# Performance work log

Measured on AMD Instinct MI355X. Metric: run time of the kernel, lower is better.

Reference implementation:

```python
import jax, jax.numpy as jnp
import numpy as np

BN_EPS = 1e-5


def _gather_neighbors(feat, idx):
    # feat: [B, N, C]; idx: [B, N, K] -> [B, N, K, C]
    B, N, C = feat.shape
    K = idx.shape[-1]
    g = jnp.take_along_axis(feat, idx.reshape(B, N * K)[:, :, None], axis=1)
    return g.reshape(B, N, K, C)


def setup_inputs() -> dict:
    key = jax.random.key(0)
    k1, k2, k3 = jax.random.split(key, 3)
    B, C, N, K, Cout = 4, 128, 4096, 16, 256
    x = jax.random.normal(k1, (B, C, N, 1), dtype=jnp.float32)
    edge_index = jax.random.randint(k2, (2, B, N, K), 0, N, dtype=jnp.int64)
    # 1x1 conv weight [Cout, 2C] (kaiming-like scale), bias zeros (per reset_parameters)
    fan_in = 2 * C
    w = jax.random.normal(k3, (Cout, 2 * C), dtype=jnp.float32) * np.sqrt(2.0 / fan_in)
    b = jnp.zeros((Cout,), dtype=jnp.float32)
    gamma = jnp.ones((Cout,), dtype=jnp.float32)
    beta = jnp.zeros((Cout,), dtype=jnp.float32)
    return {"x": x, "w": w, "b": b, "gamma": gamma, "beta": beta,
            "edge_index": edge_index}


def reference(x, w, b, gamma, beta, edge_index):
    # x: [B, C, N, 1], edge_index: [2, B, N, K]
    B, C, N, _ = x.shape
    feat = jnp.transpose(x[:, :, :, 0], (0, 2, 1))            # [B, N, C]
    x_i = _gather_neighbors(feat, edge_index[1])              # [B, N, K, C]
    x_j = _gather_neighbors(feat, edge_index[0])              # [B, N, K, C]
    h = jnp.concatenate([x_i, x_j - x_i], axis=-1)            # [B, N, K, 2C]
    # 1x1 conv == per-position matmul
    y = jnp.einsum('bnkc,oc->bnko', h, w) + b                 # [B, N, K, Cout]
    y = jax.nn.relu(y)
    # BatchNorm2d (train mode): biased stats over (B, N, K) per channel
    mean = jnp.mean(y, axis=(0, 1, 2))
    var = jnp.mean(jnp.square(y), axis=(0, 1, 2)) - jnp.square(mean)
    y = (y - mean) * jax.lax.rsqrt(var + BN_EPS) * gamma + beta
    # max over neighbors K, keepdim on last torch dim
    out = jnp.max(y, axis=2)                                  # [B, N, Cout]
    return jnp.transpose(out, (0, 2, 1))[:, :, :, None]       # [B, Cout, N, 1]
```

## Files before the change

### kernel.cpp

```cpp
#include <hip/hip_runtime.h>
#include <hip/hip_bf16.h>

#define BB 4
#define CC 128
#define TWOC 256
#define NN 4096
#define KK 16
#define COUT 256
#define NPB 32
#define BNK (BB*NN*KK)
#define K1GRID ((BB*NN)/NPB)
#define NPAIR (NPB/2)

typedef __attribute__((ext_vector_type(8))) short short8;
typedef __attribute__((ext_vector_type(4))) float f32x4;

__device__ __forceinline__ short f2bs(float f) {
  union { __hip_bfloat16 h; short s; } u;
  u.h = __float2bfloat16(f);
  return u.s;
}
__device__ __forceinline__ float bs2f(unsigned short s) {
  union { unsigned int u; float f; } v;
  v.u = ((unsigned int)s) << 16;
  return v.f;
}

__global__ void __launch_bounds__(256) k0_transpose(const float* __restrict__ x,
                                                    unsigned short* __restrict__ featbf,
                                                    float* __restrict__ gsum,
                                                    float* __restrict__ gsq) {
  __shared__ float tile[64][129];
  int b = blockIdx.x >> 6;
  int n0 = (blockIdx.x & 63) << 6;
  int t = threadIdx.x;
  if (blockIdx.x == 0) { gsum[t] = 0.f; gsq[t] = 0.f; }
#pragma unroll
  for (int i = 0; i < 32; ++i) {
    int flat = t + i * 256;
    int c = flat >> 6;
    int nl = flat & 63;
    tile[nl][c] = x[((size_t)(b * CC + c) * NN) + n0 + nl];
  }
  __syncthreads();
#pragma unroll
  for (int i = 0; i < 8; ++i) {
    int e = t + i * 256;
    int c4 = (e & 31) << 2;
    int nl = e >> 5;
    ushort4 u;
    u.x = (unsigned short)f2bs(tile[nl][c4 + 0]);
    u.y = (unsigned short)f2bs(tile[nl][c4 + 1]);
    u.z = (unsigned short)f2bs(tile[nl][c4 + 2]);
    u.w = (unsigned short)f2bs(tile[nl][c4 + 3]);
    *(ushort4*)(featbf + ((size_t)(b * NN + n0 + nl) * CC + c4)) = u;
  }
}

__global__ void __launch_bounds__(512, 4) k1_main(
    const unsigned short* __restrict__ featbf,
    const float* __restrict__ w, const float* __restrict__ bias,
    const int* __restrict__ eidx,
    unsigned short* __restrict__ nmaxh, unsigned short* __restrict__ nminh,
    float* __restrict__ gsum, float* __restrict__ gsq)
{
  __shared__ short hsh[2][32 * 256];
  const int tid = threadIdx.x;
  const int wv   = tid >> 6;
  const int lane = tid & 63;
  const int l15  = lane & 15;
  const int lhi  = lane >> 4;
  const int colbase = wv * 32;

  short8 bfrag[8][2];
#pragma unroll
  for (int t = 0; t < 8; ++t)
#pragma unroll
    for (int ct = 0; ct < 2; ++ct) {
      int col = colbase + ct * 16 + l15;
      int k0 = t * 32 + lhi * 8;
      const float* wr = w + (size_t)col * TWOC + k0;
      short8 f;
#pragma unroll
      for (int j = 0; j < 8; ++j) f[j] = f2bs(wr[j]);
      bfrag[t][ct] = f;
    }
  float biasv[2];
#pragma unroll
  for (int ct = 0; ct < 2; ++ct) biasv[ct] = bias[colbase + ct * 16 + l15];

  float cs[2] = {0.f, 0.f};
  float cq[2] = {0.f, 0.f};

  const int rr  = tid >> 4;
  const int c8  = (tid & 15) * 8;
  const int swz = (rr & 7) << 4;

  const int g0 = blockIdx.x * NPB;
  const int b  = g0 >> 12;
  const int n0 = g0 & (NN - 1);
  const unsigned short* fb = featbf + (size_t)b * NN * CC;
  const int* e0 = eidx + ((b * NN + n0) * KK + rr);
  const int* e1 = e0 + BNK;

  auto stage = [&](char* hb, uint4 Fi, uint4 Fj) {
    *(uint4*)(hb + (((rr * 256 + c8) * 2) ^ swz)) = Fi;
    uint4 d;
    unsigned int* pi = (unsigned int*)&Fi;
    unsigned int* pj = (unsigned int*)&Fj;
    unsigned int* pd = (unsigned int*)&d;
#pragma unroll
    for (int q = 0; q < 4; ++q) {
      float lo = bs2f((unsigned short)(pj[q] & 0xffff)) - bs2f((unsigned short)(pi[q] & 0xffff));
      float hi = bs2f((unsigned short)(pj[q] >> 16))    - bs2f((unsigned short)(pi[q] >> 16));
      pd[q] = ((unsigned int)(unsigned short)f2bs(lo)) |
              (((unsigned int)(unsigned short)f2bs(hi)) << 16);
    }
    *(uint4*)(hb + (((rr * 256 + 128 + c8) * 2) ^ swz)) = d;
  };

  uint4 fi, fj;

  {
    int ij = e0[0], ii = e1[0];
    uint4 Fj = *(const uint4*)(fb + (size_t)ij * CC + c8);
    uint4 Fi = *(const uint4*)(fb + (size_t)ii * CC + c8);
    stage((char*)hsh[0], Fi, Fj);
    int ij1 = e0[32], ii1 = e1[32];
    fj = *(const uint4*)(fb + (size_t)ij1 * CC + c8);
    fi = *(const uint4*)(fb + (size_t)ii1 * CC + c8);
  }
  __syncthreads();

  const int asw = (l15 & 7) << 4;

  for (int p = 0; p < NPAIR; ++p) {
    char* hb = (char*)hsh[p & 1];
    char* hn = (char*)hsh[(p & 1) ^ 1];

    int ij2 = 0, ii2 = 0;
    if (p + 2 < NPAIR) { ij2 = e0[(p + 2) * 32]; ii2 = e1[(p + 2) * 32]; }

    f32x4 acc[2][2] = {};
#pragma unroll
    for (int nl = 0; nl < 2; ++nl) {
      const int rbase = (nl * 16 + l15) * 256;
#pragma unroll
      for (int t = 0; t < 8; ++t) {
        short8 a = *(short8*)(hb + (((rbase + t * 32 + lhi * 8) * 2) ^ asw));
        acc[nl][0] = __builtin_amdgcn_mfma_f32_16x16x32_bf16(a, bfrag[t][0], acc[nl][0], 0, 0, 0);
        acc[nl][1] = __builtin_amdgcn_mfma_f32_16x16x32_bf16(a, bfrag[t][1], acc[nl][1], 0, 0, 0);
      }
    }

    if (p + 1 < NPAIR) {
      stage(hn, fi, fj);
      if (p + 2 < NPAIR) {
        fj = *(const uint4*)(fb + (size_t)ij2 * CC + c8);
        fi = *(const uint4*)(fb + (size_t)ii2 * CC + c8);
      }
    }

#pragma unroll
    for (int nl = 0; nl < 2; ++nl) {
      const int g = g0 + 2 * p + nl;
#pragma unroll
      for (int ct = 0; ct < 2; ++ct) {
        float vmax = -1e30f, vmin = 1e30f, vs = 0.f, vq = 0.f;
#pragma unroll
        for (int i = 0; i < 4; ++i) {
          float v = acc[nl][ct][i] + biasv[ct];
          v = fmaxf(v, 0.f);
          vmax = fmaxf(vmax, v);
          vmin = fminf(vmin, v);
          vs += v;
          vq += v * v;
        }
        cs[ct] += vs;
        cq[ct] += vq;
        vmax = fmaxf(vmax, __shfl_xor(vmax, 16));
        vmax = fmaxf(vmax, __shfl_xor(vmax, 32));
        vmin = fminf(vmin, __shfl_xor(vmin, 16));
        vmin = fminf(vmin, __shfl_xor(vmin, 32));
        if (lane < 16) {
          int col = colbase + ct * 16 + l15;
          nmaxh[(size_t)g * COUT + col] = (unsigned short)f2bs(vmax);
          nminh[(size_t)g * COUT + col] = (unsigned short)f2bs(vmin);
        }
      }
    }
    __syncthreads();
  }

#pragma unroll
  for (int ct = 0; ct < 2; ++ct) {
    float s = cs[ct], q = cq[ct];
    s += __shfl_xor(s, 16);  s += __shfl_xor(s, 32);
    q += __shfl_xor(q, 16);  q += __shfl_xor(q, 32);
    if (lane < 16) {
      int col = colbase + ct * 16 + l15;
      atomicAdd(&gsum[col], s);
      atomicAdd(&gsq[col], q);
    }
  }
}

__global__ void __launch_bounds__(256) k2_out(const unsigned short* __restrict__ nmaxh,
                                              const unsigned short* __restrict__ nminh,
                                              const float* __restrict__ gsum,
                                              const float* __restrict__ gsq,
                                              const float* __restrict__ gamma,
                                              const float* __restrict__ beta,
                                              float* __restrict__ out) {
  __shared__ float tile[COUT][33];
  int b = blockIdx.x >> 7;
  int n0 = (blockIdx.x & 127) << 5;
  int t = threadIdx.x;
  const float inv = 1.0f / (float)BNK;
  float mean = gsum[t] * inv;
  float var  = gsq[t] * inv - mean * mean;
  float sc = gamma[t] * rsqrtf(var + 1e-5f);
  float sh = beta[t] - mean * sc;
  const unsigned short* src = (sc >= 0.f) ? nmaxh : nminh;
#pragma unroll
  for (int rr = 0; rr < 32; ++rr) {
    size_t g = (size_t)(b * NN + n0 + rr) * COUT + t;
    tile[t][rr] = bs2f(src[g]) * sc + sh;
  }
  __syncthreads();
#pragma unroll
  for (int i = 0; i < 32; ++i) {
    int o = i * 8 + (t >> 5);
    int nl = t & 31;
    out[((size_t)(b * COUT + o) * NN) + n0 + nl] = tile[o][nl];
  }
}

extern "C" void kernel_launch(void* const* d_in, const int* in_sizes, int n_in,
                              void* d_out, int out_size, void* d_ws, size_t ws_size,
                              hipStream_t stream) {
  const float* x     = (const float*)d_in[0];
  const float* w     = (const float*)d_in[1];
  const float* bias  = (const float*)d_in[2];
  const float* gamma = (const float*)d_in[3];
  const float* beta  = (const float*)d_in[4];
  const int*   eidx  = (const int*)d_in[5];

  char* ws = (char*)d_ws;
  unsigned short* featbf = (unsigned short*)(ws);
  unsigned short* nmaxh  = (unsigned short*)(ws + 4194304);
  unsigned short* nminh  = (unsigned short*)(ws + 12582912);
  float* gsum   = (float*)(ws + 20971520);
  float* gsq    = (float*)(ws + 20972544);
  float* out = (float*)d_out;

  k0_transpose<<<256, 256, 0, stream>>>(x, featbf, gsum, gsq);
  k1_main<<<K1GRID, 512, 0, stream>>>(featbf, w, bias, eidx, nmaxh, nminh, gsum, gsq);
  k2_out<<<512, 256, 0, stream>>>(nmaxh, nminh, gsum, gsq, gamma, beta, out);
}
```

Before: 157.9 us.

## Retile main kernel into 256x128 LDS-staged MFMA tiles with prepacked bf16 weights

The main kernel is restructured. Each block now handles 16 points (256 edge rows) and one half of the output channels, with the bf16 weight half staged in LDS instead of held in registers. The weights are converted to bf16 once in the transpose kernel. Each wave computes a 64x64 tile over two K phases (x_i, then x_j−x_i) using 128KB of dynamic LDS, replacing the per-pair double-buffered loop. This raises MFMA reuse per LDS load and cuts the per-block weight conversion, but the large LDS footprint limits occupancy to one block per CU and the gather latency is no longer overlapped with compute.

New measurement: 207.6 us. 31.5% more time.

```diff
diff --git a/kernel.cpp b/kernel.cpp
--- a/kernel.cpp
+++ b/kernel.cpp
@@ -7,10 +7,9 @@
 #define NN 4096
 #define KK 16
 #define COUT 256
-#define NPB 32
 #define BNK (BB*NN*KK)
-#define K1GRID ((BB*NN)/NPB)
-#define NPAIR (NPB/2)
+#define NPB 16
+#define K1GRID (((BB*NN)/NPB)*2)
 
 typedef __attribute__((ext_vector_type(8))) short short8;
 typedef __attribute__((ext_vector_type(4))) float f32x4;
@@ -28,6 +27,8 @@
 
 __global__ void __launch_bounds__(256) k0_transpose(const float* __restrict__ x,
                                                     unsigned short* __restrict__ featbf,
+                                                    const float* __restrict__ w,
+                                                    unsigned short* __restrict__ wbf,
                                                     float* __restrict__ gsum,
                                                     float* __restrict__ gsq) {
   __shared__ float tile[64][129];
@@ -35,6 +36,7 @@
   int n0 = (blockIdx.x & 63) << 6;
   int t = threadIdx.x;
   if (blockIdx.x == 0) { gsum[t] = 0.f; gsq[t] = 0.f; }
+  wbf[blockIdx.x * 256 + t] = (unsigned short)f2bs(w[blockIdx.x * 256 + t]);
 #pragma unroll
   for (int i = 0; i < 32; ++i) {
     int flat = t + i * 256;
@@ -57,57 +59,99 @@
   }
 }
 
-__global__ void __launch_bounds__(512, 4) k1_main(
+__global__ void __launch_bounds__(512, 1) k1_main(
     const unsigned short* __restrict__ featbf,
-    const float* __restrict__ w, const float* __restrict__ bias,
+    const unsigned short* __restrict__ wbf,
+    const float* __restrict__ bias,
     const int* __restrict__ eidx,
     unsigned short* __restrict__ nmaxh, unsigned short* __restrict__ nminh,
     float* __restrict__ gsum, float* __restrict__ gsq)
 {
-  __shared__ short hsh[2][32 * 256];
-  const int tid = threadIdx.x;
+  extern __shared__ char lds[];
+  char* sB = lds;
+  char* sA = lds + 65536;
+
+  const int tid  = threadIdx.x;
+  const int lane = tid & 63;
   const int wv   = tid >> 6;
-  const int lane = tid & 63;
   const int l15  = lane & 15;
   const int lhi  = lane >> 4;
-  const int colbase = wv * 32;
-
-  short8 bfrag[8][2];
-#pragma unroll
-  for (int t = 0; t < 8; ++t)
-#pragma unroll
-    for (int ct = 0; ct < 2; ++ct) {
-      int col = colbase + ct * 16 + l15;
-      int k0 = t * 32 + lhi * 8;
-      const float* wr = w + (size_t)col * TWOC + k0;
-      short8 f;
-#pragma unroll
-      for (int j = 0; j < 8; ++j) f[j] = f2bs(wr[j]);
-      bfrag[t][ct] = f;
-    }
-  float biasv[2];
-#pragma unroll
-  for (int ct = 0; ct < 2; ++ct) biasv[ct] = bias[colbase + ct * 16 + l15];
-
-  float cs[2] = {0.f, 0.f};
-  float cq[2] = {0.f, 0.f};
-
-  const int rr  = tid >> 4;
-  const int c8  = (tid & 15) * 8;
-  const int swz = (rr & 7) << 4;
-
-  const int g0 = blockIdx.x * NPB;
-  const int b  = g0 >> 12;
-  const int n0 = g0 & (NN - 1);
+  const int wr   = wv >> 1;
+  const int wc   = wv & 1;
+
+  const int mt  = (int)blockIdx.x >> 1;
+  const int chf = (int)blockIdx.x & 1;
+  const int g0  = mt * NPB;
+  const int b   = g0 >> 12;
+  const int n0  = g0 & (NN - 1);
   const unsigned short* fb = featbf + (size_t)b * NN * CC;
-  const int* e0 = eidx + ((b * NN + n0) * KK + rr);
-  const int* e1 = e0 + BNK;
-
-  auto stage = [&](char* hb, uint4 Fi, uint4 Fj) {
-    *(uint4*)(hb + (((rr * 256 + c8) * 2) ^ swz)) = Fi;
+
+  {
+    const int col = tid >> 2;
+    const int kb  = (tid & 3) * 64;
+    const unsigned short* src = wbf + (size_t)(chf * 128 + col) * TWOC + kb;
+    const int ab = col * 512 + kb * 2;
+    const int sw = (col & 7) << 4;
+#pragma unroll
+    for (int j = 0; j < 8; ++j)
+      *(uint4*)(sB + ((ab + j * 16) ^ sw)) = *(const uint4*)((const char*)src + j * 16);
+  }
+
+  const int r0 = tid >> 4;
+  const int ch = tid & 15;
+  int idxi[8], idxj[8];
+#pragma unroll
+  for (int p = 0; p < 8; ++p) {
+    int row = r0 + 32 * p;
+    int ebase = (b * NN + n0 + (row >> 4)) * KK + (row & 15);
+    idxj[p] = eidx[ebase];
+    idxi[p] = eidx[BNK + ebase];
+  }
+  uint4 fi[8];
+#pragma unroll
+  for (int p = 0; p < 8; ++p)
+    fi[p] = *(const uint4*)(fb + (size_t)idxi[p] * CC + ch * 8);
+#pragma unroll
+  for (int p = 0; p < 8; ++p) {
+    int row = r0 + 32 * p;
+    *(uint4*)(sA + ((row * 256 + ch * 16) ^ ((row & 7) << 4))) = fi[p];
+  }
+  uint4 fj[8];
+#pragma unroll
+  for (int p = 0; p < 8; ++p)
+    fj[p] = *(const uint4*)(fb + (size_t)idxj[p] * CC + ch * 8);
+
+  __syncthreads();
+
+  f32x4 acc[4][4] = {};
+  const int asw = (l15 & 7) << 4;
+
+#pragma unroll
+  for (int kk = 0; kk < 4; ++kk) {
+    short8 a[4], bg[4];
+#pragma unroll
+    for (int rt = 0; rt < 4; ++rt) {
+      int row = wr * 64 + rt * 16 + l15;
+      a[rt] = *(short8*)(sA + ((row * 256 + kk * 64 + lhi * 16) ^ asw));
+    }
+#pragma unroll
+    for (int ct = 0; ct < 4; ++ct) {
+      int col = wc * 64 + ct * 16 + l15;
+      bg[ct] = *(short8*)(sB + ((col * 512 + kk * 64 + lhi * 16) ^ asw));
+    }
+#pragma unroll
+    for (int rt = 0; rt < 4; ++rt)
+#pragma unroll
+      for (int ct = 0; ct < 4; ++ct)
+        acc[rt][ct] = __builtin_amdgcn_mfma_f32_16x16x32_bf16(a[rt], bg[ct], acc[rt][ct], 0, 0, 0);
+  }
+  __syncthreads();
+
+#pragma unroll
+  for (int p = 0; p < 8; ++p) {
     uint4 d;
-    unsigned int* pi = (unsigned int*)&Fi;
-    unsigned int* pj = (unsigned int*)&Fj;
+    unsigned int* pi = (unsigned int*)&fi[p];
+    unsigned int* pj = (unsigned int*)&fj[p];
     unsigned int* pd = (unsigned int*)&d;
 #pragma unroll
     for (int q = 0; q < 4; ++q) {
@@ -116,89 +160,69 @@
       pd[q] = ((unsigned int)(unsigned short)f2bs(lo)) |
               (((unsigned int)(unsigned short)f2bs(hi)) << 16);
     }
-    *(uint4*)(hb + (((rr * 256 + 128 + c8) * 2) ^ swz)) = d;
-  };
-
-  uint4 fi, fj;
-
-  {
-    int ij = e0[0], ii = e1[0];
-    uint4 Fj = *(const uint4*)(fb + (size_t)ij * CC + c8);
-    uint4 Fi = *(const uint4*)(fb + (size_t)ii * CC + c8);
-    stage((char*)hsh[0], Fi, Fj);
-    int ij1 = e0[32], ii1 = e1[32];
-    fj = *(const uint4*)(fb + (size_t)ij1 * CC + c8);
-    fi = *(const uint4*)(fb + (size_t)ii1 * CC + c8);
-  }
-  __syncthreads();
-
-  const int asw = (l15 & 7) << 4;
-
-  for (int p = 0; p < NPAIR; ++p) {
-    char* hb = (char*)hsh[p & 1];
-    char* hn = (char*)hsh[(p & 1) ^ 1];
-
-    int ij2 = 0, ii2 = 0;
-    if (p + 2 < NPAIR) { ij2 = e0[(p + 2) * 32]; ii2 = e1[(p + 2) * 32]; }
-
-    f32x4 acc[2][2] = {};
-#pragma unroll
-    for (int nl = 0; nl < 2; ++nl) {
-      const int rbase = (nl * 16 + l15) * 256;
-#pragma unroll
-      for (int t = 0; t < 8; ++t) {
-        short8 a = *(short8*)(hb + (((rbase + t * 32 + lhi * 8) * 2) ^ asw));
-        acc[nl][0] = __builtin_amdgcn_mfma_f32_16x16x32_bf16(a, bfrag[t][0], acc[nl][0], 0, 0, 0);
-        acc[nl][1] = __builtin_amdgcn_mfma_f32_16x16x32_bf16(a, bfrag[t][1], acc[nl][1], 0, 0, 0);
+    int row = r0 + 32 * p;
+    *(uint4*)(sA + ((row * 256 + ch * 16) ^ ((row & 7) << 4))) = d;
+  }
+  __syncthreads();
+
+#pragma unroll
+  for (int kk = 0; kk < 4; ++kk) {
+    short8 a[4], bg[4];
+#pragma unroll
+    for (int rt = 0; rt < 4; ++rt) {
+      int row = wr * 64 + rt * 16 + l15;
+      a[rt] = *(short8*)(sA + ((row * 256 + kk * 64 + lhi * 16) ^ asw));
+    }
+#pragma unroll
+    for (int ct = 0; ct < 4; ++ct) {
+      int col = wc * 64 + ct * 16 + l15;
+      bg[ct] = *(short8*)(sB + ((col * 512 + 256 + kk * 64 + lhi * 16) ^ asw));
+    }
+#pragma unroll
+    for (int rt = 0; rt < 4; ++rt)
+#pragma unroll
+      for (int ct = 0; ct < 4; ++ct)
+        acc[rt][ct] = __builtin_amdgcn_mfma_f32_16x16x32_bf16(a[rt], bg[ct], acc[rt][ct], 0, 0, 0);
+  }
+
+  float biasv[4];
+#pragma unroll
+  for (int ct = 0; ct < 4; ++ct) biasv[ct] = bias[chf * 128 + wc * 64 + ct * 16 + l15];
+
+  float cs[4] = {0.f, 0.f, 0.f, 0.f};
+  float cq[4] = {0.f, 0.f, 0.f, 0.f};
+#pragma unroll
+  for (int rt = 0; rt < 4; ++rt) {
+    const int g = g0 + wr * 4 + rt;
+#pragma unroll
+    for (int ct = 0; ct < 4; ++ct) {
+      float vmax = -1e30f, vmin = 1e30f;
+#pragma unroll
+      for (int i = 0; i < 4; ++i) {
+        float v = fmaxf(acc[rt][ct][i] + biasv[ct], 0.f);
+        vmax = fmaxf(vmax, v);
+        vmin = fminf(vmin, v);
+        cs[ct] += v;
+        cq[ct] += v * v;
       }
-    }
-
-    if (p + 1 < NPAIR) {
-      stage(hn, fi, fj);
-      if (p + 2 < NPAIR) {
-        fj = *(const uint4*)(fb + (size_t)ij2 * CC + c8);
-        fi = *(const uint4*)(fb + (size_t)ii2 * CC + c8);
+      vmax = fmaxf(vmax, __shfl_xor(vmax, 16));
+      vmax = fmaxf(vmax, __shfl_xor(vmax, 32));
+      vmin = fminf(vmin, __shfl_xor(vmin, 16));
+      vmin = fminf(vmin, __shfl_xor(vmin, 32));
+      if (lane < 16) {
+        int col = chf * 128 + wc * 64 + ct * 16 + l15;
+        nmaxh[(size_t)g * COUT + col] = (unsigned short)f2bs(vmax);
+        nminh[(size_t)g * COUT + col] = (unsigned short)f2bs(vmin);
       }
     }
-
-#pragma unroll
-    for (int nl = 0; nl < 2; ++nl) {
-      const int g = g0 + 2 * p + nl;
-#pragma unroll
-      for (int ct = 0; ct < 2; ++ct) {
-        float vmax = -1e30f, vmin = 1e30f, vs = 0.f, vq = 0.f;
-#pragma unroll
-        for (int i = 0; i < 4; ++i) {
-          float v = acc[nl][ct][i] + biasv[ct];
-          v = fmaxf(v, 0.f);
-          vmax = fmaxf(vmax, v);
-          vmin = fminf(vmin, v);
-          vs += v;
-          vq += v * v;
-        }
-        cs[ct] += vs;
-        cq[ct] += vq;
-        vmax = fmaxf(vmax, __shfl_xor(vmax, 16));
-        vmax = fmaxf(vmax, __shfl_xor(vmax, 32));
-        vmin = fminf(vmin, __shfl_xor(vmin, 16));
-        vmin = fminf(vmin, __shfl_xor(vmin, 32));
-        if (lane < 16) {
-          int col = colbase + ct * 16 + l15;
-          nmaxh[(size_t)g * COUT + col] = (unsigned short)f2bs(vmax);
-          nminh[(size_t)g * COUT + col] = (unsigned short)f2bs(vmin);
-        }
-      }
-    }
-    __syncthreads();
-  }
-
-#pragma unroll
-  for (int ct = 0; ct < 2; ++ct) {
+  }
+#pragma unroll
+  for (int ct = 0; ct < 4; ++ct) {
     float s = cs[ct], q = cq[ct];
     s += __shfl_xor(s, 16);  s += __shfl_xor(s, 32);
     q += __shfl_xor(q, 16);  q += __shfl_xor(q, 32);
     if (lane < 16) {
-      int col = colbase + ct * 16 + l15;
+      int col = chf * 128 + wc * 64 + ct * 16 + l15;
       atomicAdd(&gsum[col], s);
       atomicAdd(&gsq[col], q);
     }
@@ -248,13 +272,14 @@
 
   char* ws = (char*)d_ws;
   unsigned short* featbf = (unsigned short*)(ws);
-  unsigned short* nmaxh  = (unsigned short*)(ws + 4194304);
-  unsigned short* nminh  = (unsigned short*)(ws + 12582912);
-  float* gsum   = (float*)(ws + 20971520);
-  float* gsq    = (float*)(ws + 20972544);
+  unsigned short* wbf    = (unsigned short*)(ws + 4194304);
+  unsigned short* nmaxh  = (unsigned short*)(ws + 4325376);
+  unsigned short* nminh  = (unsigned short*)(ws + 12713984);
+  float* gsum = (float*)(ws + 21102592);
+  float* gsq  = (float*)(ws + 21103616);
   float* out = (float*)d_out;
 
-  k0_transpose<<<256, 256, 0, stream>>>(x, featbf, gsum, gsq);
-  k1_main<<<K1GRID, 512, 0, stream>>>(featbf, w, bias, eidx, nmaxh, nminh, gsum, gsq);
+  k0_transpose<<<256, 256, 0, stream>>>(x, featbf, w, wbf, gsum, gsq);
+  k1_main<<<K1GRID, 512, 131072, stream>>>(featbf, wbf, bias, eidx, nmaxh, nminh, gsum, gsq);
   k2_out<<<512, 256, 0, stream>>>(nmaxh, nminh, gsum, gsq, gamma, beta, out);
 }
```

## Fold edge difference into weights and feed gathered rows directly to MFMA

Applied to the files above, without the earlier changes.

Rewrites the conv as W1·x_i + W2·x_j, with W1 = Wl − Wr and W2 = Wr precomputed in bf16 during the prep kernel. This removes the per-edge subtraction and the LDS staging buffer. Each lane now loads gathered feature rows from global memory straight into MFMA operand registers, double-buffered in registers, so there are no block-wide barriers. Each block handles 64 nodes with 16 lanes covering 4 nodes × 4 neighbors per MFMA tile, and launch bounds drop to 2 blocks per CU; register pressure from the operand buffers and the scattered 16-byte global gathers are the risk.

After: 206.6 us. 30.9% more time.

```diff
diff --git a/kernel.cpp b/kernel.cpp
--- a/kernel.cpp
+++ b/kernel.cpp
@@ -7,34 +7,48 @@
 #define NN 4096
 #define KK 16
 #define COUT 256
-#define NPB 32
 #define BNK (BB*NN*KK)
-#define K1GRID ((BB*NN)/NPB)
-#define NPAIR (NPB/2)
+#define NODES (BB*NN)
+#define NPB 64
+#define NGRP (NPB/4)
+#define NIT (NGRP*4)
+#define K1GRID (NODES/NPB)
 
 typedef __attribute__((ext_vector_type(8))) short short8;
 typedef __attribute__((ext_vector_type(4))) float f32x4;
 
-__device__ __forceinline__ short f2bs(float f) {
+static __device__ __forceinline__ short f2bs(float f) {
   union { __hip_bfloat16 h; short s; } u;
   u.h = __float2bfloat16(f);
   return u.s;
 }
-__device__ __forceinline__ float bs2f(unsigned short s) {
+static __device__ __forceinline__ float bs2f(unsigned short s) {
   union { unsigned int u; float f; } v;
   v.u = ((unsigned int)s) << 16;
   return v.f;
 }
 
-__global__ void __launch_bounds__(256) k0_transpose(const float* __restrict__ x,
-                                                    unsigned short* __restrict__ featbf,
-                                                    float* __restrict__ gsum,
-                                                    float* __restrict__ gsq) {
+__global__ void __launch_bounds__(256) k0_prep(const float* __restrict__ x,
+                                               unsigned short* __restrict__ featbf,
+                                               const float* __restrict__ w,
+                                               unsigned short* __restrict__ w1c,
+                                               unsigned short* __restrict__ w2c,
+                                               float* __restrict__ gsum,
+                                               float* __restrict__ gsq) {
   __shared__ float tile[64][129];
   int b = blockIdx.x >> 6;
   int n0 = (blockIdx.x & 63) << 6;
   int t = threadIdx.x;
   if (blockIdx.x == 0) { gsum[t] = 0.f; gsq[t] = 0.f; }
+  {
+    int col = blockIdx.x;
+    if (t < CC) {
+      float wl = w[col * TWOC + t];
+      float wr = w[col * TWOC + CC + t];
+      w1c[col * CC + t] = (unsigned short)f2bs(wl - wr);
+      w2c[col * CC + t] = (unsigned short)f2bs(wr);
+    }
+  }
 #pragma unroll
   for (int i = 0; i < 32; ++i) {
     int flat = t + i * 256;
@@ -57,150 +71,124 @@
   }
 }
 
-__global__ void __launch_bounds__(512, 4) k1_main(
+__global__ void __launch_bounds__(512, 2) k1_main(
     const unsigned short* __restrict__ featbf,
-    const float* __restrict__ w, const float* __restrict__ bias,
+    const unsigned short* __restrict__ w1c,
+    const unsigned short* __restrict__ w2c,
+    const float* __restrict__ bias,
     const int* __restrict__ eidx,
     unsigned short* __restrict__ nmaxh, unsigned short* __restrict__ nminh,
     float* __restrict__ gsum, float* __restrict__ gsq)
 {
-  __shared__ short hsh[2][32 * 256];
-  const int tid = threadIdx.x;
+  const int tid  = threadIdx.x;
   const int wv   = tid >> 6;
   const int lane = tid & 63;
   const int l15  = lane & 15;
   const int lhi  = lane >> 4;
   const int colbase = wv * 32;
 
-  short8 bfrag[8][2];
-#pragma unroll
-  for (int t = 0; t < 8; ++t)
+  const int g0 = blockIdx.x * NPB;
+  const int b  = g0 >> 12;
+  const unsigned short* fbb = featbf + ((size_t)b * NN) * CC;
+
+  short8 w1f[4][2], w2f[4][2];
+#pragma unroll
+  for (int t = 0; t < 4; ++t)
 #pragma unroll
     for (int ct = 0; ct < 2; ++ct) {
       int col = colbase + ct * 16 + l15;
-      int k0 = t * 32 + lhi * 8;
-      const float* wr = w + (size_t)col * TWOC + k0;
-      short8 f;
-#pragma unroll
-      for (int j = 0; j < 8; ++j) f[j] = f2bs(wr[j]);
-      bfrag[t][ct] = f;
-    }
-  float biasv[2];
-#pragma unroll
-  for (int ct = 0; ct < 2; ++ct) biasv[ct] = bias[colbase + ct * 16 + l15];
+      w1f[t][ct] = *(const short8*)(w1c + (size_t)col * CC + t * 32 + lhi * 8);
+      w2f[t][ct] = *(const short8*)(w2c + (size_t)col * CC + t * 32 + lhi * 8);
+    }
+  float biasv[2] = { bias[colbase + l15], bias[colbase + 16 + l15] };
 
   float cs[2] = {0.f, 0.f};
   float cq[2] = {0.f, 0.f};
-
-  const int rr  = tid >> 4;
-  const int c8  = (tid & 15) * 8;
-  const int swz = (rr & 7) << 4;
-
-  const int g0 = blockIdx.x * NPB;
-  const int b  = g0 >> 12;
-  const int n0 = g0 & (NN - 1);
-  const unsigned short* fb = featbf + (size_t)b * NN * CC;
-  const int* e0 = eidx + ((b * NN + n0) * KK + rr);
+  float vmax[2], vmin[2];
+
+  const int nl4 = l15 >> 2;
+  const int kq  = l15 & 3;
+  const int* e0 = eidx + ((size_t)g0 * KK + nl4 * KK + kq);
   const int* e1 = e0 + BNK;
-
-  auto stage = [&](char* hb, uint4 Fi, uint4 Fj) {
-    *(uint4*)(hb + (((rr * 256 + c8) * 2) ^ swz)) = Fi;
-    uint4 d;
-    unsigned int* pi = (unsigned int*)&Fi;
-    unsigned int* pj = (unsigned int*)&Fj;
-    unsigned int* pd = (unsigned int*)&d;
-#pragma unroll
-    for (int q = 0; q < 4; ++q) {
-      float lo = bs2f((unsigned short)(pj[q] & 0xffff)) - bs2f((unsigned short)(pi[q] & 0xffff));
-      float hi = bs2f((unsigned short)(pj[q] >> 16))    - bs2f((unsigned short)(pi[q] >> 16));
-      pd[q] = ((unsigned int)(unsigned short)f2bs(lo)) |
-              (((unsigned int)(unsigned short)f2bs(hi)) << 16);
-    }
-    *(uint4*)(hb + (((rr * 256 + 128 + c8) * 2) ^ swz)) = d;
+  auto qoff = [&](int q) { return ((q >> 2) << 6) + ((q & 3) << 2); };
+
+  int ejA, eiA, ejB, eiB;
+  short8 xiA[4], xjA[4], xiB[4], xjB[4];
+
+  ejA = e0[qoff(0)]; eiA = e1[qoff(0)];
+  ejB = e0[qoff(1)]; eiB = e1[qoff(1)];
+#pragma unroll
+  for (int t = 0; t < 4; ++t) {
+    xiA[t] = *(const short8*)(fbb + (size_t)eiA * CC + t * 32 + lhi * 8);
+    xjA[t] = *(const short8*)(fbb + (size_t)ejA * CC + t * 32 + lhi * 8);
+  }
+
+  auto body = [&](int RT, int q,
+                  int& ejC, int& eiC, short8 (&xiC)[4], short8 (&xjC)[4],
+                  int ejN, int eiN, short8 (&xiN)[4], short8 (&xjN)[4]) {
+    if (q + 2 < NIT) {
+      int o = qoff(q + 2);
+      ejC = e0[o];
+      eiC = e1[o];
+    }
+    if (q + 1 < NIT) {
+#pragma unroll
+      for (int t = 0; t < 4; ++t) {
+        xiN[t] = *(const short8*)(fbb + (size_t)eiN * CC + t * 32 + lhi * 8);
+        xjN[t] = *(const short8*)(fbb + (size_t)ejN * CC + t * 32 + lhi * 8);
+      }
+    }
+    f32x4 acc[2] = {};
+#pragma unroll
+    for (int t = 0; t < 4; ++t) {
+      acc[0] = __builtin_amdgcn_mfma_f32_16x16x32_bf16(xiC[t], w1f[t][0], acc[0], 0, 0, 0);
+      acc[1] = __builtin_amdgcn_mfma_f32_16x16x32_bf16(xiC[t], w1f[t][1], acc[1], 0, 0, 0);
+    }
+#pragma unroll
+    for (int t = 0; t < 4; ++t) {
+      acc[0] = __builtin_amdgcn_mfma_f32_16x16x32_bf16(xjC[t], w2f[t][0], acc[0], 0, 0, 0);
+      acc[1] = __builtin_amdgcn_mfma_f32_16x16x32_bf16(xjC[t], w2f[t][1], acc[1], 0, 0, 0);
+    }
+    if (RT == 0) { vmax[0] = 0.f; vmax[1] = 0.f; vmin[0] = 1e30f; vmin[1] = 1e30f; }
+#pragma unroll
+    for (int ct = 0; ct < 2; ++ct) {
+#pragma unroll
+      for (int i = 0; i < 4; ++i) {
+        float v = fmaxf(acc[ct][i] + biasv[ct], 0.f);
+        vmax[ct] = fmaxf(vmax[ct], v);
+        vmin[ct] = fminf(vmin[ct], v);
+        cs[ct] += v;
+        cq[ct] += v * v;
+      }
+    }
+    if (RT == 3) {
+      int g = g0 + ((q >> 2) << 2) + lhi;
+#pragma unroll
+      for (int ct = 0; ct < 2; ++ct) {
+        size_t o = (size_t)g * COUT + colbase + ct * 16 + l15;
+        nmaxh[o] = (unsigned short)f2bs(vmax[ct]);
+        nminh[o] = (unsigned short)f2bs(vmin[ct]);
+      }
+    }
   };
 
-  uint4 fi, fj;
-
-  {
-    int ij = e0[0], ii = e1[0];
-    uint4 Fj = *(const uint4*)(fb + (size_t)ij * CC + c8);
-    uint4 Fi = *(const uint4*)(fb + (size_t)ii * CC + c8);
-    stage((char*)hsh[0], Fi, Fj);
-    int ij1 = e0[32], ii1 = e1[32];
-    fj = *(const uint4*)(fb + (size_t)ij1 * CC + c8);
-    fi = *(const uint4*)(fb + (size_t)ii1 * CC + c8);
-  }
-  __syncthreads();
-
-  const int asw = (l15 & 7) << 4;
-
-  for (int p = 0; p < NPAIR; ++p) {
-    char* hb = (char*)hsh[p & 1];
-    char* hn = (char*)hsh[(p & 1) ^ 1];
-
-    int ij2 = 0, ii2 = 0;
-    if (p + 2 < NPAIR) { ij2 = e0[(p + 2) * 32]; ii2 = e1[(p + 2) * 32]; }
-
-    f32x4 acc[2][2] = {};
-#pragma unroll
-    for (int nl = 0; nl < 2; ++nl) {
-      const int rbase = (nl * 16 + l15) * 256;
-#pragma unroll
-      for (int t = 0; t < 8; ++t) {
-        short8 a = *(short8*)(hb + (((rbase + t * 32 + lhi * 8) * 2) ^ asw));
-        acc[nl][0] = __builtin_amdgcn_mfma_f32_16x16x32_bf16(a, bfrag[t][0], acc[nl][0], 0, 0, 0);
-        acc[nl][1] = __builtin_amdgcn_mfma_f32_16x16x32_bf16(a, bfrag[t][1], acc[nl][1], 0, 0, 0);
-      }
-    }
-
-    if (p + 1 < NPAIR) {
-      stage(hn, fi, fj);
-      if (p + 2 < NPAIR) {
-        fj = *(const uint4*)(fb + (size_t)ij2 * CC + c8);
-        fi = *(const uint4*)(fb + (size_t)ii2 * CC + c8);
-      }
-    }
-
-#pragma unroll
-    for (int nl = 0; nl < 2; ++nl) {
-      const int g = g0 + 2 * p + nl;
-#pragma unroll
-      for (int ct = 0; ct < 2; ++ct) {
-        float vmax = -1e30f, vmin = 1e30f, vs = 0.f, vq = 0.f;
-#pragma unroll
-        for (int i = 0; i < 4; ++i) {
-          float v = acc[nl][ct][i] + biasv[ct];
-          v = fmaxf(v, 0.f);
-          vmax = fmaxf(vmax, v);
-          vmin = fminf(vmin, v);
-          vs += v;
-          vq += v * v;
-        }
-        cs[ct] += vs;
-        cq[ct] += vq;
-        vmax = fmaxf(vmax, __shfl_xor(vmax, 16));
-        vmax = fmaxf(vmax, __shfl_xor(vmax, 32));
-        vmin = fminf(vmin, __shfl_xor(vmin, 16));
-        vmin = fminf(vmin, __shfl_xor(vmin, 32));
-        if (lane < 16) {
-          int col = colbase + ct * 16 + l15;
-          nmaxh[(size_t)g * COUT + col] = (unsigned short)f2bs(vmax);
-          nminh[(size_t)g * COUT + col] = (unsigned short)f2bs(vmin);
-        }
-      }
-    }
-    __syncthreads();
+  for (int grp = 0; grp < NGRP; ++grp) {
+    int q = grp << 2;
+    body(0, q,     ejA, eiA, xiA, xjA, ejB, eiB, xiB, xjB);
+    body(1, q + 1, ejB, eiB, xiB, xjB, ejA, eiA, xiA, xjA);
+    body(2, q + 2, ejA, eiA, xiA, xjA, ejB, eiB, xiB, xjB);
+    body(3, q + 3, ejB, eiB, xiB, xjB, ejA, eiA, xiA, xjA);
   }
 
 #pragma unroll
   for (int ct = 0; ct < 2; ++ct) {
-    float s = cs[ct], q = cq[ct];
-    s += __shfl_xor(s, 16);  s += __shfl_xor(s, 32);
-    q += __shfl_xor(q, 16);  q += __shfl_xor(q, 32);
+    float s = cs[ct];
+    s += __shfl_xor(s, 16); s += __shfl_xor(s, 32);
+    float qq = cq[ct];
+    qq += __shfl_xor(qq, 16); qq += __shfl_xor(qq, 32);
     if (lane < 16) {
-      int col = colbase + ct * 16 + l15;
-      atomicAdd(&gsum[col], s);
-      atomicAdd(&gsq[col], q);
+      atomicAdd(&gsum[colbase + ct * 16 + l15], s);
+      atomicAdd(&gsq[colbase + ct * 16 + l15], qq);
     }
   }
 }
@@ -248,13 +236,15 @@
 
   char* ws = (char*)d_ws;
   unsigned short* featbf = (unsigned short*)(ws);
-  unsigned short* nmaxh  = (unsigned short*)(ws + 4194304);
-  unsigned short* nminh  = (unsigned short*)(ws + 12582912);
-  float* gsum   = (float*)(ws + 20971520);
-  float* gsq    = (float*)(ws + 20972544);
+  unsigned short* w1c    = (unsigned short*)(ws + 4194304);
+  unsigned short* w2c    = (unsigned short*)(ws + 4259840);
+  unsigned short* nmaxh  = (unsigned short*)(ws + 4325376);
+  unsigned short* nminh  = (unsigned short*)(ws + 12713984);
+  float* gsum = (float*)(ws + 21102592);
+  float* gsq  = (float*)(ws + 21103616);
   float* out = (float*)d_out;
 
-  k0_transpose<<<256, 256, 0, stream>>>(x, featbf, gsum, gsq);
-  k1_main<<<K1GRID, 512, 0, stream>>>(featbf, w, bias, eidx, nmaxh, nminh, gsum, gsq);
+  k0_prep<<<256, 256, 0, stream>>>(x, featbf, w, w1c, w2c, gsum, gsq);
+  k1_main<<<K1GRID, 512, 0, stream>>>(featbf, w1c, w2c, bias, eidx, nmaxh, nminh, gsum, gsq);
   k2_out<<<512, 256, 0, stream>>>(nmaxh, nminh, gsum, gsq, gamma, beta, out);
 }
```
